# Kernel tuning notes

Measured on AMD Instinct MI355X. Metric: run time of the kernel, lower is better.

Reference implementation:

```python
import jax, jax.numpy as jnp
import numpy as np

MAX_ITERS = 20
TOL = 1e-6
STEP = 1.0
EPS = 1e-7
CLIP = 1e-7


def _normalize(x, axis=-1):
    n = jnp.linalg.norm(x, axis=axis, keepdims=True)
    return x / jnp.maximum(n, 1e-12)


def _safe_acos(x):
    return jnp.arccos(jnp.clip(x, -1.0 + CLIP, 1.0 - CLIP))


def setup_inputs() -> dict:
    key = jax.random.key(0)
    NC, K, N, D = 1000, 8, 32, 128
    X_groups = jax.random.normal(key, (NC, K, N, D), dtype=jnp.float32)
    return {"X_groups": X_groups}


def reference(X_groups):
    # X_groups: (NC, K, N, D)
    NC, K, N, D = X_groups.shape
    X = X_groups.reshape(NC * K, N, D)
    Xn = _normalize(X)                      # (G, N, D) unit vectors
    mu = _normalize(jnp.mean(Xn, axis=1))   # (G, D) init mean

    done = jnp.array(False)
    for _ in range(MAX_ITERS):
        dots = jnp.einsum('gd,gnd->gn', mu, Xn)             # (G, N)
        theta = _safe_acos(dots)
        sin_t = jnp.maximum(jnp.sin(theta), EPS)
        diff = Xn - dots[..., None] * mu[:, None, :]        # (G, N, D)
        log_vecs = (theta / sin_t)[..., None] * diff        # log map
        v = jnp.mean(log_vecs, axis=1)                      # (G, D)
        v_norm = jnp.maximum(jnp.linalg.norm(v, axis=-1, keepdims=True), EPS)
        done = done | (jnp.max(v_norm) < TOL)               # global convergence (as in torch .item() check)
        v_step = STEP * v
        vs_norm = jnp.maximum(jnp.linalg.norm(v_step, axis=-1, keepdims=True), EPS)
        mu_new = jnp.cos(vs_norm) * mu + jnp.sin(vs_norm) * (v_step / vs_norm)  # exp map
        mu_new = _normalize(mu_new)
        mu = jnp.where(done, mu, mu_new)

    # calc_cluster_distance: features (G, N, D) @ means (G, D)
    sims = jnp.einsum('gnd,gd->gn', Xn, mu)
    sims = jnp.clip(sims, -1 + CLIP, 1 - CLIP)
    loss = jnp.mean(jnp.sum(jnp.arccos(sims) ** 2, axis=-1))
    return loss
```

## Files before the change

### kernel.cpp

```cpp
#include <hip/hip_runtime.h>
#include <stdint.h>

#define MAX_ITERS 20
#define EPSV 1e-7f
#define CLIPV 1e-7f
#define PI_F 3.14159265358979f
#define PIO2_F 1.57079632679490f

typedef __attribute__((ext_vector_type(8))) short short8;
typedef __attribute__((ext_vector_type(4))) float f4;

__device__ __forceinline__ f4 mfma_bf16(short8 a, short8 b, f4 c) {
    return __builtin_amdgcn_mfma_f32_16x16x32_bf16(a, b, c, 0, 0, 0);
}

__device__ __forceinline__ float rl(float v, int l) {
    return __int_as_float(__builtin_amdgcn_readlane(__float_as_int(v), l));
}

template <int CTRL>
__device__ __forceinline__ float dpp_add(float v) {
    int p = __builtin_amdgcn_update_dpp(0, __float_as_int(v), CTRL, 0xF, 0xF, true);
    return v + __int_as_float(p);
}
template <int CTRL>
__device__ __forceinline__ float dpp_mov(float v) {
    return __int_as_float(__builtin_amdgcn_update_dpp(0, __float_as_int(v), CTRL, 0xF, 0xF, true));
}

__device__ __forceinline__ float rowsum16(float v) {
    v = dpp_add<0xB1>(v);
    v = dpp_add<0x4E>(v);
    v = dpp_add<0x141>(v);
    v = dpp_add<0x140>(v);
    return v;
}

__device__ __forceinline__ float halfsum_rl(float v, bool hB) {
    v = rowsum16(v);
    float sA = rl(v, 0) + rl(v, 16);
    float sB = rl(v, 32) + rl(v, 48);
    return hB ? sB : sA;
}

__device__ __forceinline__ float halfsum_sw(float v) {
    v = rowsum16(v);
    int sw = __builtin_amdgcn_ds_swizzle(__float_as_int(v), 0x401F);
    return v + __int_as_float(sw);
}

__device__ __forceinline__ float fast_acos(float x) {
    float a = fabsf(x);
    bool big = a > 0.5f;
    float z = big ? 0.5f * (1.0f - a) : x * x;
    float s = big ? sqrtf(z) : x;
    float p = fmaf(z, fmaf(z, fmaf(z, fmaf(z, 4.2163199048e-2f, 2.4181311049e-2f),
                                   4.5470025998e-2f), 7.4953002686e-2f),
                   1.6666752422e-1f);
    float r = fmaf(s * z, p, s);
    float big_val = (x < 0.0f) ? (PI_F - 2.0f * r) : (2.0f * r);
    return big ? big_val : (PIO2_F - r);
}

__device__ __forceinline__ void cvt_hilo(const float* v, short8& hi, short8& lo) {
#pragma unroll
    for (int i = 0; i < 8; ++i) {
        float x = v[i];
        uint32_t u = __float_as_uint(x);
        float hf = __uint_as_float(u & 0xFFFF0000u);
        float lf = x - hf;
        hi[i] = (short)(u >> 16);
        lo[i] = (short)(__float_as_uint(lf) >> 16);
    }
}

#define WSTEPA(CTRL, GI) { curA = dpp_mov<CTRL>(curA); accA = fmaf(Grow2[GI], curA, accA); }
#define WSTEPB(CTRL, GI) { curB = dpp_mov<CTRL>(curB); accB = fmaf(Grow2[(GI) + 16], curB, accB); }

__global__ void __launch_bounds__(256, 4) karcher(const float* __restrict__ X,
                                                  float* __restrict__ ws,
                                                  int n_groups) {
    __shared__ float sG[8][32 * 33];
    __shared__ float sInv[8][32];
    __shared__ float sPart[8];

    const int lane = threadIdx.x & 63;
    const int wid  = threadIdx.x >> 6;
    const int g0   = blockIdx.x * 8 + wid * 2;
    if (threadIdx.x < 8) sPart[threadIdx.x] = 0.f;
    if (g0 >= n_groups) return;

    const int col  = lane & 15;
    const int quad = lane >> 4;

#pragma unroll
    for (int gg = 0; gg < 2; ++gg) {
        if (g0 + gg >= n_groups) break;
        const float* Xg = X + (size_t)(g0 + gg) * (32 * 128);
        f4 acc00 = {0.f, 0.f, 0.f, 0.f};
        f4 acc01 = acc00, acc10 = acc00, acc11 = acc00;
#pragma unroll
        for (int kc = 0; kc < 4; ++kc) {
            const float* p0 = Xg + col * 128 + kc * 32 + quad * 8;
            const float* p1 = p0 + 16 * 128;
            float r0[8], r1[8];
            *(float4*)(r0)     = *(const float4*)(p0);
            *(float4*)(r0 + 4) = *(const float4*)(p0 + 4);
            *(float4*)(r1)     = *(const float4*)(p1);
            *(float4*)(r1 + 4) = *(const float4*)(p1 + 4);
            short8 H0, L0, H1, L1;
            cvt_hilo(r0, H0, L0);
            cvt_hilo(r1, H1, L1);
            acc00 = mfma_bf16(H0, H0, acc00);
            acc00 = mfma_bf16(H0, L0, acc00);
            acc00 = mfma_bf16(L0, H0, acc00);
            acc01 = mfma_bf16(H0, H1, acc01);
            acc01 = mfma_bf16(H0, L1, acc01);
            acc01 = mfma_bf16(L0, H1, acc01);
            acc10 = mfma_bf16(H1, H0, acc10);
            acc10 = mfma_bf16(H1, L0, acc10);
            acc10 = mfma_bf16(L1, H0, acc10);
            acc11 = mfma_bf16(H1, H1, acc11);
            acc11 = mfma_bf16(H1, L1, acc11);
            acc11 = mfma_bf16(L1, H1, acc11);
        }
        float* Gw = sG[wid * 2 + gg];
#pragma unroll
        for (int i = 0; i < 4; ++i) {
            int rw = quad * 4 + i;
            Gw[rw * 33 + col]             = acc00[i];
            Gw[rw * 33 + col + 16]        = acc01[i];
            Gw[(rw + 16) * 33 + col]      = acc10[i];
            Gw[(rw + 16) * 33 + col + 16] = acc11[i];
        }
    }
    __syncthreads();

    const int  half = lane >> 5;
    const bool hB   = half != 0;
    const int  r    = lane & 31;
    const float* Gh  = sG[wid * 2 + half];
    float*       siH = sInv[wid * 2 + half];

    float inv = 1.0f / fmaxf(sqrtf(Gh[r * 34]), 1e-12f);
    siH[r] = inv;
    __syncthreads();

    float Grow2[32];
#pragma unroll
    for (int g = 0; g < 32; ++g) {
        int j = r ^ g;
        Grow2[g] = Gh[r * 33 + j] * (inv * siH[j]);
    }

    float a = 1.0f / 32.0f;
    float ga;
    {
        float s0 = 0, s1 = 0, s2 = 0, s3 = 0;
#pragma unroll
        for (int g = 0; g < 8; ++g) {
            s0 += Grow2[g];
            s1 += Grow2[g + 8];
            s2 += Grow2[g + 16];
            s3 += Grow2[g + 24];
        }
        ga = ((s0 + s1) + (s2 + s3)) * (1.0f / 32.0f);
        float n2   = halfsum_rl(a * ga, hB);
        float inv0 = 1.0f / fmaxf(sqrtf(n2), 1e-12f);
        a  *= inv0;
        ga *= inv0;
    }

    for (int it = 0; it < MAX_ITERS; ++it) {
        float x  = fminf(fmaxf(ga, -1.0f + CLIPV), 1.0f - CLIPV);
        float th = fast_acos(x);
        float st = fmaxf(sqrtf(fmaxf(1.0f - x * x, 0.0f)), EPSV);
        float w  = __fdividef(th, st);

        int w16i = __builtin_amdgcn_ds_swizzle(__float_as_int(w), 0x401F);

        float C = halfsum_sw(w * ga);

        float curA = w;
        float accA = Grow2[0] * curA;
        WSTEPA(0xB1, 1)   WSTEPA(0x4E, 3)   WSTEPA(0xB1, 2)   WSTEPA(0x141, 6)
        WSTEPA(0xB1, 7)   WSTEPA(0x4E, 5)   WSTEPA(0xB1, 4)   WSTEPA(0x140, 12)
        WSTEPA(0xB1, 13)  WSTEPA(0x4E, 15)  WSTEPA(0xB1, 14)  WSTEPA(0x141, 10)
        WSTEPA(0xB1, 11)  WSTEPA(0x4E, 9)   WSTEPA(0xB1, 8)

        float curB = __int_as_float(w16i);
        float accB = Grow2[16] * curB;
        WSTEPB(0xB1, 1)   WSTEPB(0x4E, 3)   WSTEPB(0xB1, 2)   WSTEPB(0x141, 6)
        WSTEPB(0xB1, 7)   WSTEPB(0x4E, 5)   WSTEPB(0xB1, 4)   WSTEPB(0x140, 12)
        WSTEPB(0xB1, 13)  WSTEPB(0x4E, 15)  WSTEPB(0xB1, 14)  WSTEPB(0x141, 10)
        WSTEPB(0xB1, 11)  WSTEPB(0x4E, 9)   WSTEPB(0xB1, 8)

        float gw   = accA + accB;
        float gb   = (gw - C * ga) * (1.0f / 32.0f);
        float beta = (w  - C * a ) * (1.0f / 32.0f);

        float vv = halfsum_rl(beta * gb, hB);
        float vs = fmaxf(sqrtf(fmaxf(vv, 0.0f)), EPSV);
        float cv = __cosf(vs);
        float sv = __fdividef(__sinf(vs), vs);
        a  = fmaf(sv, beta, cv * a);
        ga = fmaf(sv, gb, cv * ga);
        if (__all(vs < 1e-6f)) break;
    }

    float xf = fminf(fmaxf(ga, -1.0f + CLIPV), 1.0f - CLIPV);
    float t  = fast_acos(xf);
    float ls = halfsum_rl(t * t, hB);
    if (r == 0 && (g0 + half) < n_groups) sPart[wid * 2 + half] = ls;
    __syncthreads();
    if (threadIdx.x == 0) {
        float s = 0.f;
#pragma unroll
        for (int i = 0; i < 8; ++i) s += sPart[i];
        ws[blockIdx.x] = s;
    }
}

__global__ void __launch_bounds__(256) reduce_partials(const float* __restrict__ ws,
                                                       float* __restrict__ out,
                                                       int n, float scale) {
    __shared__ float sred[4];
    float s = 0.f;
    for (int i = threadIdx.x; i < n; i += 256) s += ws[i];
#pragma unroll
    for (int m = 32; m >= 1; m >>= 1) s += __shfl_xor(s, m, 64);
    const int lane = threadIdx.x & 63, wid = threadIdx.x >> 6;
    if (lane == 0) sred[wid] = s;
    __syncthreads();
    if (threadIdx.x == 0)
        out[0] = ((sred[0] + sred[1]) + (sred[2] + sred[3])) * scale;
}

extern "C" void kernel_launch(void* const* d_in, const int* in_sizes, int n_in,
                              void* d_out, int out_size, void* d_ws, size_t ws_size,
                              hipStream_t stream) {
    const float* X = (const float*)d_in[0];
    float* out = (float*)d_out;
    float* ws = (float*)d_ws;
    int n_groups = in_sizes[0] / (32 * 128);
    int blocks = (n_groups + 7) / 8;
    karcher<<<blocks, 256, 0, stream>>>(X, ws, n_groups);
    reduce_partials<<<1, 256, 0, stream>>>(ws, out, blocks, 1.0f / (float)n_groups);
}
```

Measured before the change: 211.0 us.

## Split Gram computation and iteration into separate kernels with finer-grained iterate blocks

Splits the fused kernel in two. The first kernel computes the normalized Gram matrix per group with MFMA at one wave per group and writes each lane's row to global workspace. The second kernel runs the Riemannian iterations with 64-thread blocks, two groups per block, so iteration blocks schedule independently of the MFMA phase and latency is spread across more workgroups. In exchange it adds a 32 MB workspace round trip and an extra launch, and it falls back to the monolithic kernel when the workspace is too small.

```diff
diff --git a/kernel.cpp b/kernel.cpp
--- a/kernel.cpp
+++ b/kernel.cpp
@@ -77,9 +77,178 @@
 #define WSTEPA(CTRL, GI) { curA = dpp_mov<CTRL>(curA); accA = fmaf(Grow2[GI], curA, accA); }
 #define WSTEPB(CTRL, GI) { curB = dpp_mov<CTRL>(curB); accB = fmaf(Grow2[(GI) + 16], curB, accB); }
 
-__global__ void __launch_bounds__(256, 4) karcher(const float* __restrict__ X,
-                                                  float* __restrict__ ws,
-                                                  int n_groups) {
+__global__ void __launch_bounds__(256, 6) gram_norm(const float* __restrict__ X,
+                                                    float* __restrict__ gro,
+                                                    int n_groups) {
+    __shared__ float sG[4][32 * 33];
+    __shared__ float sInv[4][32];
+
+    const int lane = threadIdx.x & 63;
+    const int wid  = threadIdx.x >> 6;
+    const int g    = blockIdx.x * 4 + wid;
+    if (g >= n_groups) return;
+
+    const float* Xg = X + (size_t)g * (32 * 128);
+    const int col  = lane & 15;
+    const int quad = lane >> 4;
+
+    f4 acc00 = {0.f, 0.f, 0.f, 0.f};
+    f4 acc01 = acc00, acc10 = acc00, acc11 = acc00;
+#pragma unroll
+    for (int kc = 0; kc < 4; ++kc) {
+        const float* p0 = Xg + col * 128 + kc * 32 + quad * 8;
+        const float* p1 = p0 + 16 * 128;
+        float r0[8], r1[8];
+        *(float4*)(r0)     = *(const float4*)(p0);
+        *(float4*)(r0 + 4) = *(const float4*)(p0 + 4);
+        *(float4*)(r1)     = *(const float4*)(p1);
+        *(float4*)(r1 + 4) = *(const float4*)(p1 + 4);
+        short8 H0, L0, H1, L1;
+        cvt_hilo(r0, H0, L0);
+        cvt_hilo(r1, H1, L1);
+        acc00 = mfma_bf16(H0, H0, acc00);
+        acc00 = mfma_bf16(H0, L0, acc00);
+        acc00 = mfma_bf16(L0, H0, acc00);
+        acc01 = mfma_bf16(H0, H1, acc01);
+        acc01 = mfma_bf16(H0, L1, acc01);
+        acc01 = mfma_bf16(L0, H1, acc01);
+        acc10 = mfma_bf16(H1, H0, acc10);
+        acc10 = mfma_bf16(H1, L0, acc10);
+        acc10 = mfma_bf16(L1, H0, acc10);
+        acc11 = mfma_bf16(H1, H1, acc11);
+        acc11 = mfma_bf16(H1, L1, acc11);
+        acc11 = mfma_bf16(L1, H1, acc11);
+    }
+
+    float* Gw = sG[wid];
+#pragma unroll
+    for (int i = 0; i < 4; ++i) {
+        int rw = quad * 4 + i;
+        Gw[rw * 33 + col]             = acc00[i];
+        Gw[rw * 33 + col + 16]        = acc01[i];
+        Gw[(rw + 16) * 33 + col]      = acc10[i];
+        Gw[(rw + 16) * 33 + col + 16] = acc11[i];
+    }
+
+    const int half = lane >> 5;
+    const int r    = lane & 31;
+    float inv = 1.0f / fmaxf(sqrtf(Gw[r * 34]), 1e-12f);
+    if (lane < 32) sInv[wid][r] = inv;
+
+    float Grow2[32];
+#pragma unroll
+    for (int gg = 0; gg < 32; ++gg) {
+        int j = r ^ gg;
+        Grow2[gg] = Gw[r * 33 + j] * (inv * sInv[wid][j]);
+    }
+
+    float* dst = gro + (size_t)g * 1024 + r * 32;
+    if (half == 0) {
+        float4 t0 = {Grow2[0],  Grow2[1],  Grow2[2],  Grow2[3]};
+        float4 t1 = {Grow2[4],  Grow2[5],  Grow2[6],  Grow2[7]};
+        float4 t2 = {Grow2[8],  Grow2[9],  Grow2[10], Grow2[11]};
+        float4 t3 = {Grow2[12], Grow2[13], Grow2[14], Grow2[15]};
+        *(float4*)(dst + 0)  = t0;
+        *(float4*)(dst + 4)  = t1;
+        *(float4*)(dst + 8)  = t2;
+        *(float4*)(dst + 12) = t3;
+    } else {
+        float4 t0 = {Grow2[16], Grow2[17], Grow2[18], Grow2[19]};
+        float4 t1 = {Grow2[20], Grow2[21], Grow2[22], Grow2[23]};
+        float4 t2 = {Grow2[24], Grow2[25], Grow2[26], Grow2[27]};
+        float4 t3 = {Grow2[28], Grow2[29], Grow2[30], Grow2[31]};
+        *(float4*)(dst + 16) = t0;
+        *(float4*)(dst + 20) = t1;
+        *(float4*)(dst + 24) = t2;
+        *(float4*)(dst + 28) = t3;
+    }
+}
+
+__global__ void __launch_bounds__(64) iterate(const float* __restrict__ gro,
+                                              float* __restrict__ part,
+                                              int n_groups) {
+    const int  lane = threadIdx.x;
+    const int  half = lane >> 5;
+    const bool hB   = half != 0;
+    const int  r    = lane & 31;
+    const int  g0   = blockIdx.x * 2;
+    if (g0 >= n_groups) return;
+
+    const float* src = gro + (size_t)(g0 + half) * 1024 + r * 32;
+    float Grow2[32];
+#pragma unroll
+    for (int t = 0; t < 8; ++t) {
+        float4 v = *(const float4*)(src + t * 4);
+        Grow2[t * 4 + 0] = v.x;
+        Grow2[t * 4 + 1] = v.y;
+        Grow2[t * 4 + 2] = v.z;
+        Grow2[t * 4 + 3] = v.w;
+    }
+
+    float a = 1.0f / 32.0f;
+    float ga;
+    {
+        float s0 = 0, s1 = 0, s2 = 0, s3 = 0;
+#pragma unroll
+        for (int g = 0; g < 8; ++g) {
+            s0 += Grow2[g];
+            s1 += Grow2[g + 8];
+            s2 += Grow2[g + 16];
+            s3 += Grow2[g + 24];
+        }
+        ga = ((s0 + s1) + (s2 + s3)) * (1.0f / 32.0f);
+        float n2   = halfsum_rl(a * ga, hB);
+        float inv0 = 1.0f / fmaxf(sqrtf(n2), 1e-12f);
+        a  *= inv0;
+        ga *= inv0;
+    }
+
+    for (int it = 0; it < MAX_ITERS; ++it) {
+        float x  = fminf(fmaxf(ga, -1.0f + CLIPV), 1.0f - CLIPV);
+        float th = fast_acos(x);
+        float st = fmaxf(sqrtf(fmaxf(1.0f - x * x, 0.0f)), EPSV);
+        float w  = __fdividef(th, st);
+
+        int w16i = __builtin_amdgcn_ds_swizzle(__float_as_int(w), 0x401F);
+        float C = halfsum_sw(w * ga);
+
+        float curA = w;
+        float accA = Grow2[0] * curA;
+        WSTEPA(0xB1, 1)   WSTEPA(0x4E, 3)   WSTEPA(0xB1, 2)   WSTEPA(0x141, 6)
+        WSTEPA(0xB1, 7)   WSTEPA(0x4E, 5)   WSTEPA(0xB1, 4)   WSTEPA(0x140, 12)
+        WSTEPA(0xB1, 13)  WSTEPA(0x4E, 15)  WSTEPA(0xB1, 14)  WSTEPA(0x141, 10)
+        WSTEPA(0xB1, 11)  WSTEPA(0x4E, 9)   WSTEPA(0xB1, 8)
+
+        float curB = __int_as_float(w16i);
+        float accB = Grow2[16] * curB;
+        WSTEPB(0xB1, 1)   WSTEPB(0x4E, 3)   WSTEPB(0xB1, 2)   WSTEPB(0x141, 6)
+        WSTEPB(0xB1, 7)   WSTEPB(0x4E, 5)   WSTEPB(0xB1, 4)   WSTEPB(0x140, 12)
+        WSTEPB(0xB1, 13)  WSTEPB(0x4E, 15)  WSTEPB(0xB1, 14)  WSTEPB(0x141, 10)
+        WSTEPB(0xB1, 11)  WSTEPB(0x4E, 9)   WSTEPB(0xB1, 8)
+
+        float gw   = accA + accB;
+        float gb   = (gw - C * ga) * (1.0f / 32.0f);
+        float beta = (w  - C * a ) * (1.0f / 32.0f);
+
+        float vv = halfsum_rl(beta * gb, hB);
+        float vs = fmaxf(sqrtf(fmaxf(vv, 0.0f)), EPSV);
+        float cv = __cosf(vs);
+        float sv = __fdividef(__sinf(vs), vs);
+        a  = fmaf(sv, beta, cv * a);
+        ga = fmaf(sv, gb, cv * ga);
+        if (__all(vs < 1e-6f)) break;
+    }
+
+    float xf = fminf(fmaxf(ga, -1.0f + CLIPV), 1.0f - CLIPV);
+    float t  = fast_acos(xf);
+    float ls = halfsum_rl(t * t, hB);
+    float total = rl(ls, 0) + rl(ls, 32);
+    if (lane == 0) part[blockIdx.x] = total;
+}
+
+__global__ void __launch_bounds__(256, 4) karcher_mono(const float* __restrict__ X,
+                                                       float* __restrict__ ws,
+                                                       int n_groups) {
     __shared__ float sG[8][32 * 33];
     __shared__ float sInv[8][32];
     __shared__ float sPart[8];
@@ -176,29 +345,23 @@
         float th = fast_acos(x);
         float st = fmaxf(sqrtf(fmaxf(1.0f - x * x, 0.0f)), EPSV);
         float w  = __fdividef(th, st);
-
         int w16i = __builtin_amdgcn_ds_swizzle(__float_as_int(w), 0x401F);
-
         float C = halfsum_sw(w * ga);
-
         float curA = w;
         float accA = Grow2[0] * curA;
         WSTEPA(0xB1, 1)   WSTEPA(0x4E, 3)   WSTEPA(0xB1, 2)   WSTEPA(0x141, 6)
         WSTEPA(0xB1, 7)   WSTEPA(0x4E, 5)   WSTEPA(0xB1, 4)   WSTEPA(0x140, 12)
         WSTEPA(0xB1, 13)  WSTEPA(0x4E, 15)  WSTEPA(0xB1, 14)  WSTEPA(0x141, 10)
         WSTEPA(0xB1, 11)  WSTEPA(0x4E, 9)   WSTEPA(0xB1, 8)
-
         float curB = __int_as_float(w16i);
         float accB = Grow2[16] * curB;
         WSTEPB(0xB1, 1)   WSTEPB(0x4E, 3)   WSTEPB(0xB1, 2)   WSTEPB(0x141, 6)
         WSTEPB(0xB1, 7)   WSTEPB(0x4E, 5)   WSTEPB(0xB1, 4)   WSTEPB(0x140, 12)
         WSTEPB(0xB1, 13)  WSTEPB(0x4E, 15)  WSTEPB(0xB1, 14)  WSTEPB(0x141, 10)
         WSTEPB(0xB1, 11)  WSTEPB(0x4E, 9)   WSTEPB(0xB1, 8)
-
         float gw   = accA + accB;
         float gb   = (gw - C * ga) * (1.0f / 32.0f);
         float beta = (w  - C * a ) * (1.0f / 32.0f);
-
         float vv = halfsum_rl(beta * gb, hB);
         float vs = fmaxf(sqrtf(fmaxf(vv, 0.0f)), EPSV);
         float cv = __cosf(vs);
@@ -243,7 +406,23 @@
     float* out = (float*)d_out;
     float* ws = (float*)d_ws;
     int n_groups = in_sizes[0] / (32 * 128);
-    int blocks = (n_groups + 7) / 8;
-    karcher<<<blocks, 256, 0, stream>>>(X, ws, n_groups);
-    reduce_partials<<<1, 256, 0, stream>>>(ws, out, blocks, 1.0f / (float)n_groups);
-}
+
+    int blocksA = (n_groups + 3) / 4;
+    int blocksB = (n_groups + 1) / 2;
+    size_t need = (size_t)n_groups * 1024 * sizeof(float)
+                + (size_t)blocksB * sizeof(float);
+
+    if (ws_size >= need) {
+        float* gro  = ws;
+        float* part = ws + (size_t)n_groups * 1024;
+        gram_norm<<<blocksA, 256, 0, stream>>>(X, gro, n_groups);
+        iterate<<<blocksB, 64, 0, stream>>>(gro, part, n_groups);
+        reduce_partials<<<1, 256, 0, stream>>>(part, out, blocksB,
+                                               1.0f / (float)n_groups);
+    } else {
+        int blocks = (n_groups + 7) / 8;
+        karcher_mono<<<blocks, 256, 0, stream>>>(X, ws, n_groups);
+        reduce_partials<<<1, 256, 0, stream>>>(ws, out, blocks,
+                                               1.0f / (float)n_groups);
+    }
+}
```

Result: slower. 246.2 us (+16.7%).

## Stage group tiles via global_load_lds and process one group per wave

Applied to the files above, without the earlier changes.

Each wave now handles a single group. Its 32x128 tile is copied straight from global memory into a per-wave LDS buffer with global_load_lds, using an XOR swizzle to avoid bank conflicts, and the MFMA Gram computation reads from LDS. The same buffer is then reused for the Gram matrix, which removes the block-wide barriers and the cross-wave convergence vote. The cost is that both halves of the wave redundantly run the iterative solve for the same group, and LDS use per block grows, which lowers occupancy and doubles the number of waves needed.

```diff
diff --git a/kernel.cpp b/kernel.cpp
--- a/kernel.cpp
+++ b/kernel.cpp
@@ -36,11 +36,9 @@
     return v;
 }
 
-__device__ __forceinline__ float halfsum_rl(float v, bool hB) {
+__device__ __forceinline__ float wavesum32(float v) {
     v = rowsum16(v);
-    float sA = rl(v, 0) + rl(v, 16);
-    float sB = rl(v, 32) + rl(v, 48);
-    return hB ? sB : sA;
+    return rl(v, 0) + rl(v, 16);
 }
 
 __device__ __forceinline__ float halfsum_sw(float v) {
@@ -77,37 +75,58 @@
 #define WSTEPA(CTRL, GI) { curA = dpp_mov<CTRL>(curA); accA = fmaf(Grow2[GI], curA, accA); }
 #define WSTEPB(CTRL, GI) { curB = dpp_mov<CTRL>(curB); accB = fmaf(Grow2[(GI) + 16], curB, accB); }
 
-__global__ void __launch_bounds__(256, 4) karcher(const float* __restrict__ X,
-                                                  float* __restrict__ ws,
-                                                  int n_groups) {
-    __shared__ float sG[8][32 * 33];
-    __shared__ float sInv[8][32];
-    __shared__ float sPart[8];
+#define GLOAD_LDS16(srcp, ldsp)                                                   \
+    __builtin_amdgcn_global_load_lds(                                             \
+        (const __attribute__((address_space(1))) uint32_t*)(srcp),                \
+        (__attribute__((address_space(3))) uint32_t*)(ldsp), 16, 0, 0)
+
+__global__ void __launch_bounds__(256) karcher(const float* __restrict__ X,
+                                               float* __restrict__ ws,
+                                               int n_groups) {
+    __shared__ float stage[4][4096];
+    __shared__ float sInv[4][32];
+    __shared__ float sPart[4];
 
     const int lane = threadIdx.x & 63;
     const int wid  = threadIdx.x >> 6;
-    const int g0   = blockIdx.x * 8 + wid * 2;
-    if (threadIdx.x < 8) sPart[threadIdx.x] = 0.f;
-    if (g0 >= n_groups) return;
+    const int g    = blockIdx.x * 4 + wid;
+    if (g >= n_groups) return;
+
+    const float* Xg = X + (size_t)g * 4096;
+    {
+        const int g2  = lane & 31;
+        const int rrb = lane >> 5;
+#pragma unroll
+        for (int i = 0; i < 16; ++i) {
+            int rr  = 2 * i + rrb;
+            int g2s = g2 ^ (rr & 7);
+            const float* src = Xg + rr * 128 + g2s * 4;
+            GLOAD_LDS16(src, &stage[wid][i * 256]);
+        }
+    }
+    asm volatile("s_waitcnt vmcnt(0)" ::: "memory");
+    __builtin_amdgcn_sched_barrier(0);
 
     const int col  = lane & 15;
     const int quad = lane >> 4;
 
-#pragma unroll
-    for (int gg = 0; gg < 2; ++gg) {
-        if (g0 + gg >= n_groups) break;
-        const float* Xg = X + (size_t)(g0 + gg) * (32 * 128);
-        f4 acc00 = {0.f, 0.f, 0.f, 0.f};
-        f4 acc01 = acc00, acc10 = acc00, acc11 = acc00;
+    f4 acc00 = {0.f, 0.f, 0.f, 0.f};
+    f4 acc01 = acc00, acc10 = acc00, acc11 = acc00;
+    {
+        float* st = stage[wid];
+        const int x0 = col & 7;
+        const int b0 = col * 128;
+        const int b1 = (col + 16) * 128;
 #pragma unroll
         for (int kc = 0; kc < 4; ++kc) {
-            const float* p0 = Xg + col * 128 + kc * 32 + quad * 8;
-            const float* p1 = p0 + 16 * 128;
+            int s   = kc * 4 + quad;
+            int ga0 = ((s * 2 + 0) ^ x0) * 4;
+            int ga1 = ((s * 2 + 1) ^ x0) * 4;
             float r0[8], r1[8];
-            *(float4*)(r0)     = *(const float4*)(p0);
-            *(float4*)(r0 + 4) = *(const float4*)(p0 + 4);
-            *(float4*)(r1)     = *(const float4*)(p1);
-            *(float4*)(r1 + 4) = *(const float4*)(p1 + 4);
+            *(float4*)(r0)     = *(const float4*)(st + b0 + ga0);
+            *(float4*)(r0 + 4) = *(const float4*)(st + b0 + ga1);
+            *(float4*)(r1)     = *(const float4*)(st + b1 + ga0);
+            *(float4*)(r1 + 4) = *(const float4*)(st + b1 + ga1);
             short8 H0, L0, H1, L1;
             cvt_hilo(r0, H0, L0);
             cvt_hilo(r1, H1, L1);
@@ -124,33 +143,27 @@
             acc11 = mfma_bf16(H1, L1, acc11);
             acc11 = mfma_bf16(L1, H1, acc11);
         }
-        float* Gw = sG[wid * 2 + gg];
-#pragma unroll
-        for (int i = 0; i < 4; ++i) {
-            int rw = quad * 4 + i;
-            Gw[rw * 33 + col]             = acc00[i];
-            Gw[rw * 33 + col + 16]        = acc01[i];
-            Gw[(rw + 16) * 33 + col]      = acc10[i];
-            Gw[(rw + 16) * 33 + col + 16] = acc11[i];
-        }
-    }
-    __syncthreads();
-
-    const int  half = lane >> 5;
-    const bool hB   = half != 0;
-    const int  r    = lane & 31;
-    const float* Gh  = sG[wid * 2 + half];
-    float*       siH = sInv[wid * 2 + half];
-
-    float inv = 1.0f / fmaxf(sqrtf(Gh[r * 34]), 1e-12f);
-    siH[r] = inv;
-    __syncthreads();
+    }
+
+    float* Gw = stage[wid];
+#pragma unroll
+    for (int i = 0; i < 4; ++i) {
+        int rw = quad * 4 + i;
+        Gw[rw * 33 + col]             = acc00[i];
+        Gw[rw * 33 + col + 16]        = acc01[i];
+        Gw[(rw + 16) * 33 + col]      = acc10[i];
+        Gw[(rw + 16) * 33 + col + 16] = acc11[i];
+    }
+
+    const int r = lane & 31;
+    float inv = 1.0f / fmaxf(sqrtf(Gw[r * 34]), 1e-12f);
+    if (lane < 32) sInv[wid][r] = inv;
 
     float Grow2[32];
 #pragma unroll
-    for (int g = 0; g < 32; ++g) {
-        int j = r ^ g;
-        Grow2[g] = Gh[r * 33 + j] * (inv * siH[j]);
+    for (int gg = 0; gg < 32; ++gg) {
+        int j = r ^ gg;
+        Grow2[gg] = Gw[r * 33 + j] * (inv * sInv[wid][j]);
     }
 
     float a = 1.0f / 32.0f;
@@ -158,14 +171,14 @@
     {
         float s0 = 0, s1 = 0, s2 = 0, s3 = 0;
 #pragma unroll
-        for (int g = 0; g < 8; ++g) {
-            s0 += Grow2[g];
-            s1 += Grow2[g + 8];
-            s2 += Grow2[g + 16];
-            s3 += Grow2[g + 24];
+        for (int gg = 0; gg < 8; ++gg) {
+            s0 += Grow2[gg];
+            s1 += Grow2[gg + 8];
+            s2 += Grow2[gg + 16];
+            s3 += Grow2[gg + 24];
         }
         ga = ((s0 + s1) + (s2 + s3)) * (1.0f / 32.0f);
-        float n2   = halfsum_rl(a * ga, hB);
+        float n2   = wavesum32(a * ga);
         float inv0 = 1.0f / fmaxf(sqrtf(n2), 1e-12f);
         a  *= inv0;
         ga *= inv0;
@@ -178,7 +191,6 @@
         float w  = __fdividef(th, st);
 
         int w16i = __builtin_amdgcn_ds_swizzle(__float_as_int(w), 0x401F);
-
         float C = halfsum_sw(w * ga);
 
         float curA = w;
@@ -199,26 +211,22 @@
         float gb   = (gw - C * ga) * (1.0f / 32.0f);
         float beta = (w  - C * a ) * (1.0f / 32.0f);
 
-        float vv = halfsum_rl(beta * gb, hB);
+        float vv = wavesum32(beta * gb);
         float vs = fmaxf(sqrtf(fmaxf(vv, 0.0f)), EPSV);
         float cv = __cosf(vs);
         float sv = __fdividef(__sinf(vs), vs);
         a  = fmaf(sv, beta, cv * a);
         ga = fmaf(sv, gb, cv * ga);
-        if (__all(vs < 1e-6f)) break;
+        if (vs < 1e-6f) break;
     }
 
     float xf = fminf(fmaxf(ga, -1.0f + CLIPV), 1.0f - CLIPV);
     float t  = fast_acos(xf);
-    float ls = halfsum_rl(t * t, hB);
-    if (r == 0 && (g0 + half) < n_groups) sPart[wid * 2 + half] = ls;
+    float ls = wavesum32(t * t);
+    if (lane == 0) sPart[wid] = ls;
     __syncthreads();
-    if (threadIdx.x == 0) {
-        float s = 0.f;
-#pragma unroll
-        for (int i = 0; i < 8; ++i) s += sPart[i];
-        ws[blockIdx.x] = s;
-    }
+    if (threadIdx.x == 0)
+        ws[blockIdx.x] = (sPart[0] + sPart[1]) + (sPart[2] + sPart[3]);
 }
 
 __global__ void __launch_bounds__(256) reduce_partials(const float* __restrict__ ws,
@@ -243,7 +251,7 @@
     float* out = (float*)d_out;
     float* ws = (float*)d_ws;
     int n_groups = in_sizes[0] / (32 * 128);
-    int blocks = (n_groups + 7) / 8;
+    int blocks = (n_groups + 3) / 4;
     karcher<<<blocks, 256, 0, stream>>>(X, ws, n_groups);
     reduce_partials<<<1, 256, 0, stream>>>(ws, out, blocks, 1.0f / (float)n_groups);
 }
```

Result: slower. 217.2 us (+2.9%).

## Stage group rows into LDS via global_load_lds with XOR swizzle and double buffering

Applied to the files above, without the earlier changes.

Replaces direct global float4 loads for the Gram-matrix MFMA with asynchronous global-to-LDS copies into a swizzled per-wave buffer, alternating two 4 KB slots. The Gram matrix is then written into the same LDS with an XOR-swizzled layout instead of the padded 33-stride layout. This drops the block-wide __syncthreads and shrinks LDS use. Each stage is followed by a full vmcnt(0) wait, so there is little real overlap. The per-group bounds checks for the second group and the sPart zeroing are removed, which assumes n_groups is a multiple of 8.

```diff
diff --git a/kernel.cpp b/kernel.cpp
--- a/kernel.cpp
+++ b/kernel.cpp
@@ -77,80 +77,137 @@
 #define WSTEPA(CTRL, GI) { curA = dpp_mov<CTRL>(curA); accA = fmaf(Grow2[GI], curA, accA); }
 #define WSTEPB(CTRL, GI) { curB = dpp_mov<CTRL>(curB); accB = fmaf(Grow2[(GI) + 16], curB, accB); }
 
+#define GLOAD_LDS16(srcp, ldsp)                                                   \
+    __builtin_amdgcn_global_load_lds(                                             \
+        (const __attribute__((address_space(1))) uint32_t*)(srcp),                \
+        (__attribute__((address_space(3))) uint32_t*)(ldsp), 16, 0, 0)
+
+__device__ __forceinline__ int gidx(int row, int j) {
+    return row * 32 + ((((j >> 2) ^ (row & 7)) << 2) | (j & 3));
+}
+
 __global__ void __launch_bounds__(256, 4) karcher(const float* __restrict__ X,
                                                   float* __restrict__ ws,
                                                   int n_groups) {
-    __shared__ float sG[8][32 * 33];
-    __shared__ float sInv[8][32];
+    __shared__ float lds[4][2048];
+    __shared__ float sInv[4][64];
     __shared__ float sPart[8];
 
     const int lane = threadIdx.x & 63;
     const int wid  = threadIdx.x >> 6;
     const int g0   = blockIdx.x * 8 + wid * 2;
-    if (threadIdx.x < 8) sPart[threadIdx.x] = 0.f;
     if (g0 >= n_groups) return;
 
     const int col  = lane & 15;
     const int quad = lane >> 4;
 
-#pragma unroll
-    for (int gg = 0; gg < 2; ++gg) {
-        if (g0 + gg >= n_groups) break;
-        const float* Xg = X + (size_t)(g0 + gg) * (32 * 128);
-        f4 acc00 = {0.f, 0.f, 0.f, 0.f};
-        f4 acc01 = acc00, acc10 = acc00, acc11 = acc00;
-#pragma unroll
-        for (int kc = 0; kc < 4; ++kc) {
-            const float* p0 = Xg + col * 128 + kc * 32 + quad * 8;
-            const float* p1 = p0 + 16 * 128;
-            float r0[8], r1[8];
-            *(float4*)(r0)     = *(const float4*)(p0);
-            *(float4*)(r0 + 4) = *(const float4*)(p0 + 4);
-            *(float4*)(r1)     = *(const float4*)(p1);
-            *(float4*)(r1 + 4) = *(const float4*)(p1 + 4);
-            short8 H0, L0, H1, L1;
-            cvt_hilo(r0, H0, L0);
-            cvt_hilo(r1, H1, L1);
-            acc00 = mfma_bf16(H0, H0, acc00);
-            acc00 = mfma_bf16(H0, L0, acc00);
-            acc00 = mfma_bf16(L0, H0, acc00);
-            acc01 = mfma_bf16(H0, H1, acc01);
-            acc01 = mfma_bf16(H0, L1, acc01);
-            acc01 = mfma_bf16(L0, H1, acc01);
-            acc10 = mfma_bf16(H1, H0, acc10);
-            acc10 = mfma_bf16(H1, L0, acc10);
-            acc10 = mfma_bf16(L1, H0, acc10);
-            acc11 = mfma_bf16(H1, H1, acc11);
-            acc11 = mfma_bf16(H1, L1, acc11);
-            acc11 = mfma_bf16(L1, H1, acc11);
+    float* slotA = lds[wid];
+    float* slotB = lds[wid] + 1024;
+
+    const int rrl = lane >> 3;
+    const int g2l = lane & 7;
+    auto stage = [&](const float* Xg, int kq, float* slot) {
+#pragma unroll
+        for (int i = 0; i < 4; ++i) {
+            int rr  = i * 8 + rrl;
+            int g2s = g2l ^ (rr & 7);
+            GLOAD_LDS16(Xg + rr * 128 + kq * 32 + g2s * 4, slot + i * 256);
         }
-        float* Gw = sG[wid * 2 + gg];
+    };
+
+    const int x0 = col & 7;
+    const int b0 = col * 32;
+    const int b1 = (col + 16) * 32;
+    f4 a00 = {0.f, 0.f, 0.f, 0.f}, a01 = a00, a10 = a00, a11 = a00;
+    auto gramq = [&](const float* st) {
+        int s0 = ((quad * 2 + 0) ^ x0) * 4;
+        int s1 = ((quad * 2 + 1) ^ x0) * 4;
+        float r0[8], r1[8];
+        *(float4*)(r0)     = *(const float4*)(st + b0 + s0);
+        *(float4*)(r0 + 4) = *(const float4*)(st + b0 + s1);
+        *(float4*)(r1)     = *(const float4*)(st + b1 + s0);
+        *(float4*)(r1 + 4) = *(const float4*)(st + b1 + s1);
+        short8 H0, L0, H1, L1;
+        cvt_hilo(r0, H0, L0);
+        cvt_hilo(r1, H1, L1);
+        a00 = mfma_bf16(H0, H0, a00);
+        a00 = mfma_bf16(H0, L0, a00);
+        a00 = mfma_bf16(L0, H0, a00);
+        a01 = mfma_bf16(H0, H1, a01);
+        a01 = mfma_bf16(H0, L1, a01);
+        a01 = mfma_bf16(L0, H1, a01);
+        a10 = mfma_bf16(H1, H0, a10);
+        a10 = mfma_bf16(H1, L0, a10);
+        a10 = mfma_bf16(L1, H0, a10);
+        a11 = mfma_bf16(H1, H1, a11);
+        a11 = mfma_bf16(H1, L1, a11);
+        a11 = mfma_bf16(L1, H1, a11);
+    };
+
+    auto writeG = [&](float* Gs) {
 #pragma unroll
         for (int i = 0; i < 4; ++i) {
             int rw = quad * 4 + i;
-            Gw[rw * 33 + col]             = acc00[i];
-            Gw[rw * 33 + col + 16]        = acc01[i];
-            Gw[(rw + 16) * 33 + col]      = acc10[i];
-            Gw[(rw + 16) * 33 + col + 16] = acc11[i];
+            Gs[gidx(rw,      col)]      = a00[i];
+            Gs[gidx(rw,      col + 16)] = a01[i];
+            Gs[gidx(rw + 16, col)]      = a10[i];
+            Gs[gidx(rw + 16, col + 16)] = a11[i];
         }
-    }
-    __syncthreads();
+    };
+
+#define WAIT_VM0() do {                                   \
+        asm volatile("s_waitcnt vmcnt(0)" ::: "memory");  \
+        __builtin_amdgcn_sched_barrier(0);                \
+    } while (0)
+
+    {
+        const float* Xg = X + (size_t)g0 * 4096;
+        stage(Xg, 0, slotA);
+        WAIT_VM0();
+        gramq(slotA);
+        stage(Xg, 1, slotB);
+        WAIT_VM0();
+        gramq(slotB);
+        stage(Xg, 2, slotA);
+        WAIT_VM0();
+        gramq(slotA);
+        stage(Xg, 3, slotB);
+        WAIT_VM0();
+        gramq(slotB);
+        writeG(slotA);
+    }
+    {
+        const float* Xg = X + (size_t)(g0 + 1) * 4096;
+        a00 = {0.f, 0.f, 0.f, 0.f}; a01 = a00; a10 = a00; a11 = a00;
+        stage(Xg, 0, slotB);
+        WAIT_VM0();
+        gramq(slotB);
+        stage(Xg, 1, slotB);
+        WAIT_VM0();
+        gramq(slotB);
+        stage(Xg, 2, slotB);
+        WAIT_VM0();
+        gramq(slotB);
+        stage(Xg, 3, slotB);
+        WAIT_VM0();
+        gramq(slotB);
+        writeG(slotB);
+    }
 
     const int  half = lane >> 5;
     const bool hB   = half != 0;
     const int  r    = lane & 31;
-    const float* Gh  = sG[wid * 2 + half];
-    float*       siH = sInv[wid * 2 + half];
-
-    float inv = 1.0f / fmaxf(sqrtf(Gh[r * 34]), 1e-12f);
-    siH[r] = inv;
-    __syncthreads();
+    const float* Gh = lds[wid] + half * 1024;
+
+    float inv = 1.0f / fmaxf(sqrtf(Gh[gidx(r, r)]), 1e-12f);
+    sInv[wid][lane] = inv;
+    const float* sI = sInv[wid] + half * 32;
 
     float Grow2[32];
 #pragma unroll
-    for (int g = 0; g < 32; ++g) {
-        int j = r ^ g;
-        Grow2[g] = Gh[r * 33 + j] * (inv * siH[j]);
+    for (int gg = 0; gg < 32; ++gg) {
+        int j = r ^ gg;
+        Grow2[gg] = Gh[gidx(r, j)] * (inv * sI[j]);
     }
 
     float a = 1.0f / 32.0f;
@@ -158,11 +215,11 @@
     {
         float s0 = 0, s1 = 0, s2 = 0, s3 = 0;
 #pragma unroll
-        for (int g = 0; g < 8; ++g) {
-            s0 += Grow2[g];
-            s1 += Grow2[g + 8];
-            s2 += Grow2[g + 16];
-            s3 += Grow2[g + 24];
+        for (int gg = 0; gg < 8; ++gg) {
+            s0 += Grow2[gg];
+            s1 += Grow2[gg + 8];
+            s2 += Grow2[gg + 16];
+            s3 += Grow2[gg + 24];
         }
         ga = ((s0 + s1) + (s2 + s3)) * (1.0f / 32.0f);
         float n2   = halfsum_rl(a * ga, hB);
@@ -178,7 +235,6 @@
         float w  = __fdividef(th, st);
 
         int w16i = __builtin_amdgcn_ds_swizzle(__float_as_int(w), 0x401F);
-
         float C = halfsum_sw(w * ga);
 
         float curA = w;
@@ -211,7 +267,7 @@
     float xf = fminf(fmaxf(ga, -1.0f + CLIPV), 1.0f - CLIPV);
     float t  = fast_acos(xf);
     float ls = halfsum_rl(t * t, hB);
-    if (r == 0 && (g0 + half) < n_groups) sPart[wid * 2 + half] = ls;
+    if (r == 0) sPart[wid * 2 + half] = ls;
     __syncthreads();
     if (threadIdx.x == 0) {
         float s = 0.f;
```

After: 211.1 us. About the same (+0.0%).
